# Kernel optimization log

Hardware: AMD Instinct MI355X
Metric: run time of the kernel (lower is better)

Reference implementation:

```python
import jax, jax.numpy as jnp
import numpy as np

WS = 7  # window_size
HEADS = 12
HEAD_DIM = 32
HIDDEN = 384
INNER = HEADS * HEAD_DIM


def _relative_position_index(ws):
    coords = np.stack(np.meshgrid(np.arange(ws), np.arange(ws), indexing='ij'))  # (2, ws, ws)
    flat = coords.reshape(2, -1)  # (2, ws*ws)
    rel = flat[:, :, None] - flat[:, None, :]  # (2, N, N)
    rel = rel.transpose(1, 2, 0).copy()
    rel[:, :, 0] += ws - 1
    rel[:, :, 1] += ws - 1
    rel[:, :, 0] *= 2 * ws - 1
    return rel.sum(-1)  # (N, N) int


def setup_inputs() -> dict:
    key = jax.random.key(0)
    k1, k2, k3, k4, k5 = jax.random.split(key, 5)
    x = jax.random.normal(k1, (32, 56, 56, HIDDEN), dtype=jnp.float32)
    w_qkv = jax.random.normal(k2, (HIDDEN, INNER * 3), dtype=jnp.float32) * (HIDDEN ** -0.5)
    w_out = jax.random.normal(k3, (INNER, HIDDEN), dtype=jnp.float32) * (INNER ** -0.5)
    b_out = jax.random.normal(k4, (HIDDEN,), dtype=jnp.float32) * 0.02
    bias_table = jax.random.normal(k5, ((2 * WS - 1) * (2 * WS - 1), HEADS), dtype=jnp.float32) * 0.02
    return {"x": x, "w_qkv": w_qkv, "w_out": w_out, "b_out": b_out, "bias_table": bias_table}


def _window_attention(x, w_qkv, w_out, b_out, bias_table):
    b, n_h, n_w, _ = x.shape
    ws, h, d = WS, HEADS, HEAD_DIM
    nw_h, nw_w = n_h // ws, n_w // ws
    N = ws * ws

    qkv = x @ w_qkv  # (b, n_h, n_w, 3*inner)
    q, k, v = jnp.split(qkv, 3, axis=-1)

    def to_windows(t):
        # (b, n_h, n_w, h*d) -> (b, h, nw_h*nw_w, ws*ws, d)
        t = t.reshape(b, nw_h, ws, nw_w, ws, h, d)
        t = t.transpose(0, 5, 1, 3, 2, 4, 6)
        return t.reshape(b, h, nw_h * nw_w, N, d)

    q, k, v = map(to_windows, (q, k, v))
    scale = d ** -0.5
    dots = jnp.einsum('bhwid,bhwjd->bhwij', q, k) * scale
    attn = jax.nn.softmax(dots, axis=-1)

    rel_idx = jnp.asarray(_relative_position_index(ws))  # (N, N)
    bias = bias_table[rel_idx.reshape(-1)].reshape(N, N, h)  # gather
    bias = bias.transpose(2, 0, 1)  # (h, N, N)
    # NOTE: faithful to source — bias added AFTER softmax
    attn = attn + bias[None, :, None, :, :]

    out = jnp.einsum('bhwij,bhwjd->bhwid', attn, v)  # (b, h, nw, N, d)
    out = out.reshape(b, h, nw_h, nw_w, ws, ws, d)
    out = out.transpose(0, 2, 4, 3, 5, 1, 6).reshape(b, n_h, n_w, h * d)
    return out @ w_out + b_out


def reference(x, w_qkv, w_out, b_out, bias_table):
    return _window_attention(x, w_qkv, w_out, b_out, bias_table)
```

## Files before the change

kernel.cpp:

```cpp
#include <hip/hip_runtime.h>
#include <hip/hip_bf16.h>
#include <cstdint>

#define TOK 100352
#define HID 384
#define NQKV 1152
#define NHEADS 12
#define HDIM 32

typedef __attribute__((ext_vector_type(8))) short bhalf8;
typedef __attribute__((ext_vector_type(4))) float f32x4;

__device__ __forceinline__ ushort f2bf(float f) {
  uint32_t u = __float_as_uint(f);
  return (ushort)((u + 0x7FFFu + ((u >> 16) & 1u)) >> 16);
}

__device__ __forceinline__ void gload_lds16(const ushort* g, ushort* l) {
  __builtin_amdgcn_global_load_lds(
      (const __attribute__((address_space(1))) unsigned int*)g,
      (__attribute__((address_space(3))) unsigned int*)l, 16, 0, 0);
}

__global__ __launch_bounds__(256)
void cvt_bf16(const float* __restrict__ in, ushort* __restrict__ out, const int n8) {
  const int i = blockIdx.x * 256 + threadIdx.x;
  if (i >= n8) return;
  const float4 f0 = ((const float4*)in)[(size_t)i * 2];
  const float4 f1 = ((const float4*)in)[(size_t)i * 2 + 1];
  bhalf8 v;
  v[0] = (short)f2bf(f0.x); v[1] = (short)f2bf(f0.y);
  v[2] = (short)f2bf(f0.z); v[3] = (short)f2bf(f0.w);
  v[4] = (short)f2bf(f1.x); v[5] = (short)f2bf(f1.y);
  v[6] = (short)f2bf(f1.z); v[7] = (short)f2bf(f1.w);
  ((bhalf8*)out)[i] = v;
}

__global__ __launch_bounds__(256)
void transpose_cvt(const float* __restrict__ in, ushort* __restrict__ out,
                   const int R, const int C) {
  const int i = blockIdx.x * 256 + threadIdx.x;
  if (i >= R * C) return;
  const int r = i % R, c = i / R;
  out[i] = f2bf(in[(size_t)r * C + c]);
}

__global__ __launch_bounds__(256)
void expand_bias(const float* __restrict__ bt, float* __restrict__ bx) {
  const int i = blockIdx.x * 256 + threadIdx.x;
  if (i >= NHEADS * 49 * 49) return;
  const int head = i / 2401, rc = i % 2401, r = rc / 49, c = rc % 49;
  const int idx = (r / 7 - c / 7 + 6) * 13 + (r % 7 - c % 7 + 6);
  bx[i] = bt[idx * NHEADS + head];
}

template<bool OUT_F32_BIAS>
__global__ __launch_bounds__(512)
void gemm_bt(const ushort* __restrict__ A, const ushort* __restrict__ Bt,
             const float* __restrict__ bias, void* __restrict__ Cp,
             const int N, const int K, const int nbx)
{
  __shared__ ushort As[128 * 64];
  __shared__ ushort Bs[128 * 64];

  const int tid = threadIdx.x;
  const int lane = tid & 63;
  const int wave = tid >> 6;
  const int wr = wave >> 1;
  const int wc = wave & 1;
  const int l15 = lane & 15, l16 = lane >> 4;

  int bid = blockIdx.x;
  const int nwg = gridDim.x;
  if ((nwg & 7) == 0) bid = (bid & 7) * (nwg >> 3) + (bid >> 3);
  const int row0 = (bid / nbx) * 128;
  const int col0 = (bid % nbx) * 128;

  f32x4 acc[2][4] = {};

  for (int ko = 0; ko < K; ko += 64) {
    if (ko) __syncthreads();
    #pragma unroll
    for (int it = 0; it < 2; ++it) {
      const int chunk = it * 8 + wave;
      const int idx = chunk * 64 + lane;
      const int m = idx >> 3;
      const int k8 = (((idx & 7) ^ (m & 7)) * 8);
      gload_lds16(A + (size_t)(row0 + m) * K + ko + k8, &As[chunk * 512]);
      gload_lds16(Bt + (size_t)(col0 + m) * K + ko + k8, &Bs[chunk * 512]);
    }
    __syncthreads();
    #pragma unroll
    for (int kk = 0; kk < 64; kk += 32) {
      bhalf8 af[2], bfr[4];
      const int kb = (kk + l16 * 8) * 2;
      #pragma unroll
      for (int f = 0; f < 2; ++f) {
        const int ra = wr * 32 + f * 16 + l15;
        af[f] = *(const bhalf8*)((const char*)As + ra * 128 + (kb ^ ((ra & 7) << 4)));
      }
      #pragma unroll
      for (int f = 0; f < 4; ++f) {
        const int rb = wc * 64 + f * 16 + l15;
        bfr[f] = *(const bhalf8*)((const char*)Bs + rb * 128 + (kb ^ ((rb & 7) << 4)));
      }
      #pragma unroll
      for (int fm = 0; fm < 2; ++fm)
        #pragma unroll
        for (int fn = 0; fn < 4; ++fn)
          acc[fm][fn] = __builtin_amdgcn_mfma_f32_16x16x32_bf16(af[fm], bfr[fn], acc[fm][fn], 0, 0, 0);
    }
  }

  #pragma unroll
  for (int fm = 0; fm < 2; ++fm) {
    const int rb = row0 + wr * 32 + fm * 16 + l16 * 4;
    #pragma unroll
    for (int fn = 0; fn < 4; ++fn) {
      const int cc = col0 + wc * 64 + fn * 16 + l15;
      const float badd = OUT_F32_BIAS ? bias[cc] : 0.f;
      #pragma unroll
      for (int i = 0; i < 4; ++i) {
        const float vv = acc[fm][fn][i] + badd;
        if (OUT_F32_BIAS) ((float*)Cp)[(size_t)(rb + i) * N + cc] = vv;
        else ((ushort*)Cp)[(size_t)(rb + i) * N + cc] = f2bf(vv);
      }
    }
  }
}

__global__ __launch_bounds__(256)
void win_attn2(const ushort* __restrict__ qkv, const float* __restrict__ biasx,
               ushort* __restrict__ attn_out)
{
  __shared__ ushort VtAll[4][32 * 64];
  __shared__ ushort PsAll[4][64 * 64];

  const int tid = threadIdx.x;
  const int lane = tid & 63, wave = tid >> 6;
  const int l15 = lane & 15, l16 = lane >> 4;
  const int gid = blockIdx.x * 4 + wave;
  const int head = gid % NHEADS;
  const int win = gid / NHEADS;
  const int b = win >> 6, wi = (win >> 3) & 7, wj = win & 7;
  char* Vt = (char*)VtAll[wave];
  char* Ps = (char*)PsAll[wave];

  const int base_row = b * 3136 + wi * 7 * 56 + wj * 7;

  #pragma unroll
  for (int it = 0; it < 4; ++it) {
    const int t = lane;
    const int d0 = it * 8;
    bhalf8 v = {0, 0, 0, 0, 0, 0, 0, 0};
    if (t < 49) {
      const size_t off = (size_t)(base_row + (t / 7) * 56 + (t % 7)) * NQKV
                         + 768 + head * HDIM + d0;
      v = *(const bhalf8*)(qkv + off);
    }
    #pragma unroll
    for (int j = 0; j < 8; ++j) {
      const int d = d0 + j;
      const int byteoff = ((d * 64 + t) * 2) ^ ((d & 7) << 4);
      *(ushort*)(Vt + byteoff) = (ushort)v[j];
    }
  }

  bhalf8 qf[4], kf[4];
  #pragma unroll
  for (int f = 0; f < 4; ++f) {
    const int r = f * 16 + l15;
    const int rr = r < 49 ? r : 48;
    const size_t off = (size_t)(base_row + (rr / 7) * 56 + (rr % 7)) * NQKV
                       + head * HDIM + l16 * 8;
    qf[f] = *(const bhalf8*)(qkv + off);
    kf[f] = *(const bhalf8*)(qkv + off + 384);
  }

  const f32x4 fz = {};
  f32x4 s[4][4];
  #pragma unroll
  for (int fm = 0; fm < 4; ++fm)
    #pragma unroll
    for (int fn = 0; fn < 4; ++fn)
      s[fm][fn] = __builtin_amdgcn_mfma_f32_16x16x32_bf16(qf[fm], kf[fn], fz, 0, 0, 0);

  const float scale = 0.17677669529663687f;
  const int colv[4] = {l15, 16 + l15, 32 + l15, 48 + l15};
  const float* brow_base = biasx + (size_t)head * 2401;

  #pragma unroll
  for (int fm = 0; fm < 4; ++fm) {
    #pragma unroll
    for (int i = 0; i < 4; ++i) {
      const int r = fm * 16 + l16 * 4 + i;
      float val[4];
      float mx = -1e30f;
      #pragma unroll
      for (int fn = 0; fn < 4; ++fn) {
        val[fn] = s[fm][fn][i] * scale;
        if (colv[fn] < 49) mx = fmaxf(mx, val[fn]);
      }
      #pragma unroll
      for (int off = 1; off < 16; off <<= 1) mx = fmaxf(mx, __shfl_xor(mx, off));
      float e[4]; float sum = 0.f;
      #pragma unroll
      for (int fn = 0; fn < 4; ++fn) {
        e[fn] = (colv[fn] < 49) ? __expf(val[fn] - mx) : 0.f;
        sum += e[fn];
      }
      #pragma unroll
      for (int off = 1; off < 16; off <<= 1) sum += __shfl_xor(sum, off);
      const float inv = 1.f / sum;
      const float* brow = brow_base + r * 49;
      #pragma unroll
      for (int fn = 0; fn < 4; ++fn) {
        const int c = colv[fn];
        float a = 0.f;
        if (r < 49 && c < 49) a = e[fn] * inv + brow[c];
        const int byteoff = ((r * 64 + c) * 2) ^ ((r & 7) << 4);
        *(ushort*)(Ps + byteoff) = f2bf(a);
      }
    }
  }

  f32x4 o[4][2] = {};
  #pragma unroll
  for (int kk = 0; kk < 64; kk += 32) {
    bhalf8 pf[4], vf[2];
    #pragma unroll
    for (int f = 0; f < 4; ++f) {
      const int r = f * 16 + l15;
      pf[f] = *(const bhalf8*)(Ps + (((r * 64 + kk + l16 * 8) * 2) ^ ((r & 7) << 4)));
    }
    #pragma unroll
    for (int f = 0; f < 2; ++f) {
      const int d = f * 16 + l15;
      vf[f] = *(const bhalf8*)(Vt + (((d * 64 + kk + l16 * 8) * 2) ^ ((d & 7) << 4)));
    }
    #pragma unroll
    for (int fm = 0; fm < 4; ++fm)
      #pragma unroll
      for (int fn = 0; fn < 2; ++fn)
        o[fm][fn] = __builtin_amdgcn_mfma_f32_16x16x32_bf16(pf[fm], vf[fn], o[fm][fn], 0, 0, 0);
  }

  #pragma unroll
  for (int fm = 0; fm < 4; ++fm) {
    #pragma unroll
    for (int i = 0; i < 4; ++i) {
      const int r = fm * 16 + l16 * 4 + i;
      if (r < 49) {
        const int grow = base_row + (r / 7) * 56 + (r % 7);
        #pragma unroll
        for (int fn = 0; fn < 2; ++fn) {
          const int d = fn * 16 + l15;
          attn_out[(size_t)grow * HID + head * HDIM + d] = f2bf(o[fm][fn][i]);
        }
      }
    }
  }
}

extern "C" void kernel_launch(void* const* d_in, const int* in_sizes, int n_in,
                              void* d_out, int out_size, void* d_ws, size_t ws_size,
                              hipStream_t stream) {
  const float* x          = (const float*)d_in[0];
  const float* w_qkv      = (const float*)d_in[1];
  const float* w_out      = (const float*)d_in[2];
  const float* b_out      = (const float*)d_in[3];
  const float* bias_table = (const float*)d_in[4];
  float* out = (float*)d_out;

  ushort* xb     = (ushort*)d_ws;
  ushort* qkv    = xb + (size_t)TOK * HID;
  ushort* wqkvT  = qkv + (size_t)TOK * NQKV;
  ushort* woutT  = wqkvT + (size_t)NQKV * HID;
  float*  biasx  = (float*)(woutT + (size_t)HID * HID);
  ushort* attn_o = xb;

  {
    const int n8 = TOK * HID / 8;
    cvt_bf16<<<dim3((n8 + 255) / 256), dim3(256), 0, stream>>>(x, xb, n8);
    transpose_cvt<<<dim3(HID * NQKV / 256), dim3(256), 0, stream>>>(w_qkv, wqkvT, HID, NQKV);
    transpose_cvt<<<dim3(HID * HID / 256), dim3(256), 0, stream>>>(w_out, woutT, HID, HID);
    expand_bias<<<dim3((NHEADS * 2401 + 255) / 256), dim3(256), 0, stream>>>(bias_table, biasx);
  }

  gemm_bt<false><<<dim3((NQKV / 128) * (TOK / 128)), dim3(512), 0, stream>>>(
      xb, wqkvT, nullptr, qkv, NQKV, HID, NQKV / 128);

  win_attn2<<<dim3(2048 * NHEADS / 4), dim3(256), 0, stream>>>(qkv, biasx, attn_o);

  gemm_bt<true><<<dim3((HID / 128) * (TOK / 128)), dim3(512), 0, stream>>>(
      attn_o, woutT, b_out, out, HID, HID, HID / 128);
}
```

Baseline: 372.9 us.

## Fuse fp32-to-bf16 input conversion into QKV GEMM with larger row tile

Removes the standalone cvt_bf16 kernel and has the QKV GEMM load fp32 x directly, converting it to bf16 in registers before writing swizzled LDS. The QKV GEMM tile grows from 128x128 to 256x128 (4x4 MFMA fragments per wave), so each block reuses the B tile across more rows. This drops a full write and re-read of the bf16 copy of x. In exchange, A is now loaded through registers instead of async global-to-LDS copies, which adds register pressure and may expose load latency.

```diff
diff --git a/kernel.cpp b/kernel.cpp
--- a/kernel.cpp
+++ b/kernel.cpp
@@ -20,20 +20,6 @@
   __builtin_amdgcn_global_load_lds(
       (const __attribute__((address_space(1))) unsigned int*)g,
       (__attribute__((address_space(3))) unsigned int*)l, 16, 0, 0);
-}
-
-__global__ __launch_bounds__(256)
-void cvt_bf16(const float* __restrict__ in, ushort* __restrict__ out, const int n8) {
-  const int i = blockIdx.x * 256 + threadIdx.x;
-  if (i >= n8) return;
-  const float4 f0 = ((const float4*)in)[(size_t)i * 2];
-  const float4 f1 = ((const float4*)in)[(size_t)i * 2 + 1];
-  bhalf8 v;
-  v[0] = (short)f2bf(f0.x); v[1] = (short)f2bf(f0.y);
-  v[2] = (short)f2bf(f0.z); v[3] = (short)f2bf(f0.w);
-  v[4] = (short)f2bf(f1.x); v[5] = (short)f2bf(f1.y);
-  v[6] = (short)f2bf(f1.z); v[7] = (short)f2bf(f1.w);
-  ((bhalf8*)out)[i] = v;
 }
 
 __global__ __launch_bounds__(256)
@@ -54,40 +40,115 @@
   bx[i] = bt[idx * NHEADS + head];
 }
 
-template<bool OUT_F32_BIAS>
 __global__ __launch_bounds__(512)
-void gemm_bt(const ushort* __restrict__ A, const ushort* __restrict__ Bt,
-             const float* __restrict__ bias, void* __restrict__ Cp,
-             const int N, const int K, const int nbx)
+void gemm_x_qkv(const float* __restrict__ X, const ushort* __restrict__ Bt,
+                ushort* __restrict__ C)
 {
-  __shared__ ushort As[128 * 64];
+  __shared__ ushort As[256 * 64];
   __shared__ ushort Bs[128 * 64];
 
   const int tid = threadIdx.x;
-  const int lane = tid & 63;
-  const int wave = tid >> 6;
+  const int lane = tid & 63, wave = tid >> 6;
   const int wr = wave >> 1;
   const int wc = wave & 1;
   const int l15 = lane & 15, l16 = lane >> 4;
 
   int bid = blockIdx.x;
   const int nwg = gridDim.x;
-  if ((nwg & 7) == 0) bid = (bid & 7) * (nwg >> 3) + (bid >> 3);
-  const int row0 = (bid / nbx) * 128;
-  const int col0 = (bid % nbx) * 128;
-
-  f32x4 acc[2][4] = {};
-
-  for (int ko = 0; ko < K; ko += 64) {
+  bid = (bid & 7) * (nwg >> 3) + (bid >> 3);
+  const int row0 = (bid / 9) * 256;
+  const int col0 = (bid % 9) * 128;
+
+  f32x4 acc[4][4] = {};
+
+  for (int ko = 0; ko < HID; ko += 64) {
     if (ko) __syncthreads();
     #pragma unroll
     for (int it = 0; it < 2; ++it) {
       const int chunk = it * 8 + wave;
       const int idx = chunk * 64 + lane;
       const int m = idx >> 3;
-      const int k8 = (((idx & 7) ^ (m & 7)) * 8);
-      gload_lds16(A + (size_t)(row0 + m) * K + ko + k8, &As[chunk * 512]);
-      gload_lds16(Bt + (size_t)(col0 + m) * K + ko + k8, &Bs[chunk * 512]);
+      const int k8 = ((idx & 7) ^ (m & 7)) * 8;
+      gload_lds16(Bt + (size_t)(col0 + m) * HID + ko + k8, &Bs[chunk * 512]);
+    }
+    #pragma unroll
+    for (int a = 0; a < 4; ++a) {
+      const int idx = a * 512 + tid;
+      const int m = idx >> 3;
+      const int k8 = (idx & 7) * 8;
+      const float* g = X + (size_t)(row0 + m) * HID + ko + k8;
+      const float4 f0 = *(const float4*)g;
+      const float4 f1 = *(const float4*)(g + 4);
+      bhalf8 v;
+      v[0] = (short)f2bf(f0.x); v[1] = (short)f2bf(f0.y);
+      v[2] = (short)f2bf(f0.z); v[3] = (short)f2bf(f0.w);
+      v[4] = (short)f2bf(f1.x); v[5] = (short)f2bf(f1.y);
+      v[6] = (short)f2bf(f1.z); v[7] = (short)f2bf(f1.w);
+      *(bhalf8*)((char*)As + m * 128 + ((k8 * 2) ^ ((m & 7) << 4))) = v;
+    }
+    __syncthreads();
+    #pragma unroll
+    for (int kk = 0; kk < 64; kk += 32) {
+      const int kb = (kk + l16 * 8) * 2;
+      bhalf8 af[4], bfr[4];
+      #pragma unroll
+      for (int f = 0; f < 4; ++f) {
+        const int ra = wr * 64 + f * 16 + l15;
+        const int rb = wc * 64 + f * 16 + l15;
+        af[f]  = *(const bhalf8*)((const char*)As + ra * 128 + (kb ^ ((ra & 7) << 4)));
+        bfr[f] = *(const bhalf8*)((const char*)Bs + rb * 128 + (kb ^ ((rb & 7) << 4)));
+      }
+      #pragma unroll
+      for (int fm = 0; fm < 4; ++fm)
+        #pragma unroll
+        for (int fn = 0; fn < 4; ++fn)
+          acc[fm][fn] = __builtin_amdgcn_mfma_f32_16x16x32_bf16(af[fm], bfr[fn], acc[fm][fn], 0, 0, 0);
+    }
+  }
+
+  #pragma unroll
+  for (int fm = 0; fm < 4; ++fm) {
+    const int rb = row0 + wr * 64 + fm * 16 + l16 * 4;
+    #pragma unroll
+    for (int fn = 0; fn < 4; ++fn) {
+      const int cc = col0 + wc * 64 + fn * 16 + l15;
+      #pragma unroll
+      for (int i = 0; i < 4; ++i)
+        C[(size_t)(rb + i) * NQKV + cc] = f2bf(acc[fm][fn][i]);
+    }
+  }
+}
+
+__global__ __launch_bounds__(512)
+void gemm_attn_out(const ushort* __restrict__ A, const ushort* __restrict__ Bt,
+                   const float* __restrict__ bias, float* __restrict__ Cp)
+{
+  __shared__ ushort As[128 * 64];
+  __shared__ ushort Bs[128 * 64];
+
+  const int tid = threadIdx.x;
+  const int lane = tid & 63, wave = tid >> 6;
+  const int wr = wave >> 1, wc = wave & 1;
+  const int l15 = lane & 15, l16 = lane >> 4;
+
+  int bid = blockIdx.x;
+  const int nwg = gridDim.x;
+  bid = (bid & 7) * (nwg >> 3) + (bid >> 3);
+  const int row0 = (bid / 3) * 128;
+  const int col0 = (bid % 3) * 128;
+
+  f32x4 acc[2][4] = {};
+
+  for (int ko = 0; ko < HID; ko += 64) {
+    if (ko) __syncthreads();
+    #pragma unroll
+    for (int it = 0; it < 2; ++it) {
+      const int chunk = it * 8 + wave;
+      const int idx = chunk * 64 + lane;
+      const int m = idx >> 3;
+      const int k8 = ((idx & 7) ^ (m & 7)) * 8;
+      gload_lds16(A + (size_t)(row0 + m) * HID + ko + k8, &As[chunk * 512]);
+      gload_lds16(Bt + (size_t)(col0 + m) * HID + ko + k8, &Bs[chunk * 512]);
     }
     __syncthreads();
     #pragma unroll
@@ -118,13 +179,10 @@
     #pragma unroll
     for (int fn = 0; fn < 4; ++fn) {
       const int cc = col0 + wc * 64 + fn * 16 + l15;
-      const float badd = OUT_F32_BIAS ? bias[cc] : 0.f;
-      #pragma unroll
-      for (int i = 0; i < 4; ++i) {
-        const float vv = acc[fm][fn][i] + badd;
-        if (OUT_F32_BIAS) ((float*)Cp)[(size_t)(rb + i) * N + cc] = vv;
-        else ((ushort*)Cp)[(size_t)(rb + i) * N + cc] = f2bf(vv);
-      }
+      const float badd = bias[cc];
+      #pragma unroll
+      for (int i = 0; i < 4; ++i)
+        Cp[(size_t)(rb + i) * HID + cc] = acc[fm][fn][i] + badd;
     }
   }
 }
@@ -272,26 +330,20 @@
   const float* bias_table = (const float*)d_in[4];
   float* out = (float*)d_out;
 
-  ushort* xb     = (ushort*)d_ws;
-  ushort* qkv    = xb + (size_t)TOK * HID;
+  ushort* attn_o = (ushort*)d_ws;
+  ushort* qkv    = attn_o + (size_t)TOK * HID;
   ushort* wqkvT  = qkv + (size_t)TOK * NQKV;
   ushort* woutT  = wqkvT + (size_t)NQKV * HID;
   float*  biasx  = (float*)(woutT + (size_t)HID * HID);
-  ushort* attn_o = xb;
-
-  {
-    const int n8 = TOK * HID / 8;
-    cvt_bf16<<<dim3((n8 + 255) / 256), dim3(256), 0, stream>>>(x, xb, n8);
-    transpose_cvt<<<dim3(HID * NQKV / 256), dim3(256), 0, stream>>>(w_qkv, wqkvT, HID, NQKV);
-    transpose_cvt<<<dim3(HID * HID / 256), dim3(256), 0, stream>>>(w_out, woutT, HID, HID);
-    expand_bias<<<dim3((NHEADS * 2401 + 255) / 256), dim3(256), 0, stream>>>(bias_table, biasx);
-  }
-
-  gemm_bt<false><<<dim3((NQKV / 128) * (TOK / 128)), dim3(512), 0, stream>>>(
-      xb, wqkvT, nullptr, qkv, NQKV, HID, NQKV / 128);
+
+  transpose_cvt<<<dim3(HID * NQKV / 256), dim3(256), 0, stream>>>(w_qkv, wqkvT, HID, NQKV);
+  transpose_cvt<<<dim3(HID * HID / 256), dim3(256), 0, stream>>>(w_out, woutT, HID, HID);
+  expand_bias<<<dim3((NHEADS * 2401 + 255) / 256), dim3(256), 0, stream>>>(bias_table, biasx);
+
+  gemm_x_qkv<<<dim3((TOK / 256) * (NQKV / 128)), dim3(512), 0, stream>>>(x, wqkvT, qkv);
 
   win_attn2<<<dim3(2048 * NHEADS / 4), dim3(256), 0, stream>>>(qkv, biasx, attn_o);
 
-  gemm_bt<true><<<dim3((HID / 128) * (TOK / 128)), dim3(512), 0, stream>>>(
-      attn_o, woutT, b_out, out, HID, HID, HID / 128);
-}
+  gemm_attn_out<<<dim3((TOK / 128) * (HID / 128)), dim3(512), 0, stream>>>(
+      attn_o, woutT, b_out, out);
+}
```

Result: slower. 440.6 us (+18.2%).

## Double-buffer LDS tiles in GEMM with prefetch two stages ahead

Applied to the files above, without the earlier changes.

Splits the GEMM's shared-memory A/B tiles into two buffers and issues global-to-LDS loads for the next K tile while the current one is being multiplied. Explicit vmcnt/lgkmcnt waits and barriers replace the old single-buffer sync pattern, so memory latency can overlap with MFMA work. This doubles LDS use to 64KB per block, which may reduce occupancy. It also adds an extra barrier per iteration.

```diff
diff --git a/kernel.cpp b/kernel.cpp
--- a/kernel.cpp
+++ b/kernel.cpp
@@ -60,14 +60,12 @@
              const float* __restrict__ bias, void* __restrict__ Cp,
              const int N, const int K, const int nbx)
 {
-  __shared__ ushort As[128 * 64];
-  __shared__ ushort Bs[128 * 64];
+  __shared__ ushort As[2][128 * 64];
+  __shared__ ushort Bs[2][128 * 64];
 
   const int tid = threadIdx.x;
-  const int lane = tid & 63;
-  const int wave = tid >> 6;
-  const int wr = wave >> 1;
-  const int wc = wave & 1;
+  const int lane = tid & 63, wave = tid >> 6;
+  const int wr = wave >> 1, wc = wave & 1;
   const int l15 = lane & 15, l16 = lane >> 4;
 
   int bid = blockIdx.x;
@@ -78,18 +76,20 @@
 
   f32x4 acc[2][4] = {};
 
-  for (int ko = 0; ko < K; ko += 64) {
-    if (ko) __syncthreads();
+  auto stage = [&](int buf, int ko) {
     #pragma unroll
     for (int it = 0; it < 2; ++it) {
       const int chunk = it * 8 + wave;
       const int idx = chunk * 64 + lane;
       const int m = idx >> 3;
-      const int k8 = (((idx & 7) ^ (m & 7)) * 8);
-      gload_lds16(A + (size_t)(row0 + m) * K + ko + k8, &As[chunk * 512]);
-      gload_lds16(Bt + (size_t)(col0 + m) * K + ko + k8, &Bs[chunk * 512]);
-    }
-    __syncthreads();
+      const int k8 = ((idx & 7) ^ (m & 7)) * 8;
+      gload_lds16(A + (size_t)(row0 + m) * K + ko + k8, &As[buf][chunk * 512]);
+      gload_lds16(Bt + (size_t)(col0 + m) * K + ko + k8, &Bs[buf][chunk * 512]);
+    }
+  };
+  auto compute = [&](int buf) {
+    const char* pA = (const char*)As[buf];
+    const char* pB = (const char*)Bs[buf];
     #pragma unroll
     for (int kk = 0; kk < 64; kk += 32) {
       bhalf8 af[2], bfr[4];
@@ -97,12 +97,12 @@
       #pragma unroll
       for (int f = 0; f < 2; ++f) {
         const int ra = wr * 32 + f * 16 + l15;
-        af[f] = *(const bhalf8*)((const char*)As + ra * 128 + (kb ^ ((ra & 7) << 4)));
+        af[f] = *(const bhalf8*)(pA + ra * 128 + (kb ^ ((ra & 7) << 4)));
       }
       #pragma unroll
       for (int f = 0; f < 4; ++f) {
         const int rb = wc * 64 + f * 16 + l15;
-        bfr[f] = *(const bhalf8*)((const char*)Bs + rb * 128 + (kb ^ ((rb & 7) << 4)));
+        bfr[f] = *(const bhalf8*)(pB + rb * 128 + (kb ^ ((rb & 7) << 4)));
       }
       #pragma unroll
       for (int fm = 0; fm < 2; ++fm)
@@ -110,6 +110,28 @@
         for (int fn = 0; fn < 4; ++fn)
           acc[fm][fn] = __builtin_amdgcn_mfma_f32_16x16x32_bf16(af[fm], bfr[fn], acc[fm][fn], 0, 0, 0);
     }
+  };
+
+  const int nt = K >> 6;
+  stage(0, 0);
+  stage(1, 64);
+  asm volatile("s_waitcnt vmcnt(4)" ::: "memory");
+  __builtin_amdgcn_sched_barrier(0);
+  __builtin_amdgcn_s_barrier();
+
+  for (int t = 0; t < nt; ++t) {
+    compute(t & 1);
+    asm volatile("s_waitcnt lgkmcnt(0)" ::: "memory");
+    __builtin_amdgcn_sched_barrier(0);
+    __builtin_amdgcn_s_barrier();
+    if (t + 2 < nt) {
+      stage(t & 1, (t + 2) * 64);
+      asm volatile("s_waitcnt vmcnt(4)" ::: "memory");
+    } else {
+      asm volatile("s_waitcnt vmcnt(0)" ::: "memory");
+    }
+    __builtin_amdgcn_sched_barrier(0);
+    __builtin_amdgcn_s_barrier();
   }
 
   #pragma unroll
```

Result: no change. 375.5 us (+0.7%).
